# Kernel optimization log

Measured on AMD Instinct MI355X. Metric: run time of the kernel, lower is better.

The kernel has to match this reference:

```python
import jax, jax.numpy as jnp
import numpy as np

# module hyper-parameters (init_kwargs)
DELTA_VAR = 0.75
DELTA_DIST = 2.0
ALPHA, BETA, GAMMA = 1.0, 1.0, 0.001

B, E, H, W, C = 4, 16, 512, 512, 24


def _safe_norm(x, axis):
    # L2 norm with zero (not nan) gradient at 0, matching torch.norm's subgradient
    sq = jnp.sum(x * x, axis=axis)
    safe = jnp.where(sq == 0, 1.0, sq)
    return jnp.where(sq == 0, 0.0, jnp.sqrt(safe))


def setup_inputs() -> dict:
    key = jax.random.key(0)
    k1, k2 = jax.random.split(key)
    input_ = jax.random.normal(k1, (B, E, H, W), dtype=jnp.float32)
    target = jax.random.randint(k2, (B, 1, H, W), 0, C)  # consecutive labels 0..C-1 (w.h.p. all present)
    return {"input_": input_, "target": target, "n_instances": C}


def reference(input_, target, n_instances):
    # Discriminative loss (De Brabandere et al. 2017), math identical to the torch
    # one-hot-expansion version but expressed as segment reductions + gathers.
    Cn = int(n_instances)
    b, e = input_.shape[0], input_.shape[1]
    emb = input_.reshape(b, e, -1).transpose(0, 2, 1)  # (B, N, E)
    tgt = target.reshape(b, -1)                        # (B, N) int labels

    # per-instance cluster means: segment-sum over pixels (the torch code does the
    # same reduction via a dense BxCxExHxW one-hot expansion)
    def _means(e_bn, t_n):
        sums = jax.ops.segment_sum(e_bn, t_n, num_segments=Cn)                      # (C, E)
        counts = jax.ops.segment_sum(jnp.ones(t_n.shape, e_bn.dtype), t_n, num_segments=Cn)  # (C,)
        return sums / counts[:, None], counts

    mu, counts = jax.vmap(_means)(emb, tgt)            # (B, C, E), (B, C)

    # variance term: hinged distance of each pixel embedding to its own cluster mean
    mu_per_pix = jnp.take_along_axis(mu, tgt[:, :, None], axis=1)  # (B, N, E)
    dist = _safe_norm(emb - mu_per_pix, axis=-1)                   # (B, N)
    hinge = jnp.square(jnp.maximum(dist - DELTA_VAR, 0.0))
    var_per_inst = jax.vmap(lambda h, t: jax.ops.segment_sum(h, t, num_segments=Cn))(hinge, tgt) / counts  # (B, C)
    variance_term = jnp.mean(jnp.sum(var_per_inst, axis=1) / Cn)

    # distance term: hinged pairwise repulsion between cluster means
    dmat = _safe_norm(mu[:, :, None, :] - mu[:, None, :, :], axis=-1)  # (B, C, C)
    repulsion = 2.0 * DELTA_DIST * (1.0 - jnp.eye(Cn, dtype=mu.dtype))
    hinged = jnp.square(jnp.maximum(repulsion - dmat, 0.0))
    distance_term = jnp.mean(jnp.sum(hinged, axis=(1, 2))) / (Cn * (Cn - 1))

    # regularizer: mean norm of cluster means
    reg_term = jnp.mean(jnp.sum(_safe_norm(mu, axis=-1), axis=1)) / Cn

    return ALPHA * variance_term + BETA * distance_term + GAMMA * reg_term
```

## Files before the change

### kernel.cpp

```cpp
#include <hip/hip_runtime.h>
#include <cstdint>

#define B_SZ   4
#define E_DIM  16
#define C_INST 24
#define HW_N   262144
#define NG     (HW_N / 4)

#define DELTA_VAR  0.75f
#define DELTA_DIST 2.0f
#define ALPHA_W 1.0f
#define BETA_W  1.0f
#define GAMMA_W 0.001f

#define P1_NB   32
#define P1_ITER (NG / (P1_NB * 256))
#define CNT_PL  8
#define P2_BX   256
#define P2_TOTAL (P2_BX * B_SZ)

__global__ __launch_bounds__(256) void pass1_kernel(
    const float* __restrict__ input, const int* __restrict__ target,
    float* __restrict__ sums, float* __restrict__ counts)
{
    __shared__ float buk[C_INST][256];
    __shared__ float crow[4][C_INST];
    const int tid   = threadIdx.x;
    const int lane  = tid & 63;
    const int wv    = tid >> 6;
    const int chunk = blockIdx.x;
    const int eg    = blockIdx.y;
    const int b     = blockIdx.z;

    #pragma unroll
    for (int c = 0; c < C_INST; ++c) buk[c][tid] = 0.f;

    const int4* __restrict__ tgt4 = (const int4*)(target + (size_t)b * HW_N);
    const float4* __restrict__ src4 =
        (const float4*)(input + ((size_t)b * E_DIM + eg) * HW_N);
    const int gbase = chunk * 256 * P1_ITER + tid;

    int scnt[C_INST];
    #pragma unroll
    for (int c = 0; c < C_INST; ++c) scnt[c] = 0;

    int4   lab0 = tgt4[gbase];
    float4 x0   = src4[gbase];
    int4   lab1 = tgt4[gbase + 256];
    float4 x1   = src4[gbase + 256];
    #pragma unroll
    for (int it = 0; it < P1_ITER; ++it) {
        const int4   lc = lab0;
        const float4 xc = x0;
        lab0 = lab1; x0 = x1;
        if (it + 2 < P1_ITER) {
            lab1 = tgt4[gbase + (it + 2) * 256];
            x1   = src4[gbase + (it + 2) * 256];
        }
        buk[lc.x][tid] += xc.x;
        buk[lc.y][tid] += xc.y;
        buk[lc.z][tid] += xc.z;
        buk[lc.w][tid] += xc.w;
        if (eg < CNT_PL && it == eg) {
            #pragma unroll
            for (int c = 0; c < C_INST; ++c) {
                scnt[c] += (int)__popcll(__ballot(lc.x == c))
                         + (int)__popcll(__ballot(lc.y == c))
                         + (int)__popcll(__ballot(lc.z == c))
                         + (int)__popcll(__ballot(lc.w == c));
            }
        }
    }
    if (lane == 0) {
        #pragma unroll
        for (int c = 0; c < C_INST; ++c) crow[wv][c] = (float)scnt[c];
    }
    __syncthreads();

    if (tid < 8 * C_INST) {
        const int c  = tid >> 3;
        const int r0 = tid & 7;
        float s = 0.f;
        #pragma unroll
        for (int k = 0; k < 32; ++k)
            s += buk[c][r0 + 8 * ((k + c) & 31)];
        s += __shfl_xor(s, 1, 64);
        s += __shfl_xor(s, 2, 64);
        s += __shfl_xor(s, 4, 64);
        if (r0 == 0)
            unsafeAtomicAdd(&sums[((size_t)b * E_DIM + eg) * C_INST + c], s);
    }
    if (eg < CNT_PL && tid < C_INST) {
        const float s = crow[0][tid] + crow[1][tid] + crow[2][tid] + crow[3][tid];
        unsafeAtomicAdd(&counts[b * C_INST + tid], s);
    }
}

__global__ __launch_bounds__(256) void pass2_kernel(
    const float* __restrict__ input, const int* __restrict__ target,
    const float* __restrict__ sums, const float* __restrict__ counts,
    float* __restrict__ partials)
{
    __shared__ float4 mu4[C_INST][5];
    __shared__ float w_l[C_INST];
    __shared__ float redw[4];
    const int tid  = threadIdx.x;
    const int lane = tid & 63;
    const int wv   = tid >> 6;
    const int b    = blockIdx.y;

    if (tid < C_INST) {
        const float cv = counts[b * C_INST + tid];
        w_l[tid] = (cv > 0.f) ? 1.f / cv : 0.f;
    }
    __syncthreads();
    for (int i = tid; i < E_DIM * C_INST; i += 256) {
        const int e = i / C_INST, c = i % C_INST;
        ((float*)&mu4[c][0])[e] =
            sums[((size_t)b * E_DIM + e) * C_INST + c] * w_l[c];
    }
    __syncthreads();

    const int g = blockIdx.x * 256 + tid;
    const int4 lab4 = ((const int4*)(target + (size_t)b * HW_N))[g];
    const float4* __restrict__ src4 =
        (const float4*)(input + (size_t)b * E_DIM * NG * 4);

    float4 xv[E_DIM];
    #pragma unroll
    for (int e = 0; e < E_DIM; ++e)
        xv[e] = src4[(size_t)e * NG + g];

    float d2[4] = {0.f, 0.f, 0.f, 0.f};
    #pragma unroll
    for (int e4 = 0; e4 < 4; ++e4) {
        const float4 mx = mu4[lab4.x][e4];
        const float4 my = mu4[lab4.y][e4];
        const float4 mz = mu4[lab4.z][e4];
        const float4 mw = mu4[lab4.w][e4];
        float df;
        df = xv[4*e4+0].x - mx.x; d2[0] = fmaf(df, df, d2[0]);
        df = xv[4*e4+1].x - mx.y; d2[0] = fmaf(df, df, d2[0]);
        df = xv[4*e4+2].x - mx.z; d2[0] = fmaf(df, df, d2[0]);
        df = xv[4*e4+3].x - mx.w; d2[0] = fmaf(df, df, d2[0]);
        df = xv[4*e4+0].y - my.x; d2[1] = fmaf(df, df, d2[1]);
        df = xv[4*e4+1].y - my.y; d2[1] = fmaf(df, df, d2[1]);
        df = xv[4*e4+2].y - my.z; d2[1] = fmaf(df, df, d2[1]);
        df = xv[4*e4+3].y - my.w; d2[1] = fmaf(df, df, d2[1]);
        df = xv[4*e4+0].z - mz.x; d2[2] = fmaf(df, df, d2[2]);
        df = xv[4*e4+1].z - mz.y; d2[2] = fmaf(df, df, d2[2]);
        df = xv[4*e4+2].z - mz.z; d2[2] = fmaf(df, df, d2[2]);
        df = xv[4*e4+3].z - mz.w; d2[2] = fmaf(df, df, d2[2]);
        df = xv[4*e4+0].w - mw.x; d2[3] = fmaf(df, df, d2[3]);
        df = xv[4*e4+1].w - mw.y; d2[3] = fmaf(df, df, d2[3]);
        df = xv[4*e4+2].w - mw.z; d2[3] = fmaf(df, df, d2[3]);
        df = xv[4*e4+3].w - mw.w; d2[3] = fmaf(df, df, d2[3]);
    }

    float vloc = 0.f;
    {
        const int lp[4] = {lab4.x, lab4.y, lab4.z, lab4.w};
        #pragma unroll
        for (int p = 0; p < 4; ++p) {
            const float h = fmaxf(sqrtf(d2[p]) - DELTA_VAR, 0.f);
            vloc = fmaf(h * h, w_l[lp[p]], vloc);
        }
    }
    #pragma unroll
    for (int m = 1; m < 64; m <<= 1) vloc += __shfl_xor(vloc, m, 64);
    if (lane == 0) redw[wv] = vloc;
    __syncthreads();
    if (tid == 0)
        partials[b * P2_BX + blockIdx.x] = redw[0] + redw[1] + redw[2] + redw[3];
}

__global__ __launch_bounds__(256) void final_kernel(
    const float* __restrict__ sums, const float* __restrict__ counts,
    const float* __restrict__ partials, float* __restrict__ out)
{
    __shared__ float mu[B_SZ][C_INST][E_DIM];
    __shared__ float red[256];
    const int tid = threadIdx.x;

    for (int i = tid; i < B_SZ * C_INST * E_DIM; i += 256) {
        const int b = i / (C_INST * E_DIM);
        const int r = i % (C_INST * E_DIM);
        const int e = r / C_INST, c = r % C_INST;
        const float cv = counts[b * C_INST + c];
        mu[b][c][e] = (cv > 0.f)
            ? sums[((size_t)b * E_DIM + e) * C_INST + c] / cv : 0.f;
    }
    __syncthreads();

    float acc = 0.f;
    #pragma unroll
    for (int i = 0; i < P2_TOTAL / 256; ++i)
        acc += partials[i * 256 + tid] * (ALPHA_W / (B_SZ * C_INST));
    for (int i = tid; i < B_SZ * C_INST; i += 256) {
        const int b = i / C_INST, c = i % C_INST;
        float n2 = 0.f;
        #pragma unroll
        for (int e = 0; e < E_DIM; ++e) n2 += mu[b][c][e] * mu[b][c][e];
        acc += GAMMA_W * sqrtf(n2) * (1.0f / (B_SZ * C_INST));
    }
    for (int i = tid; i < B_SZ * C_INST * C_INST; i += 256) {
        const int b  = i / (C_INST * C_INST);
        const int r  = i % (C_INST * C_INST);
        const int c1 = r / C_INST, c2 = r % C_INST;
        if (c1 != c2) {
            float d2 = 0.f;
            #pragma unroll
            for (int e = 0; e < E_DIM; ++e) {
                const float d = mu[b][c1][e] - mu[b][c2][e];
                d2 += d * d;
            }
            const float h = fmaxf(2.0f * DELTA_DIST - sqrtf(d2), 0.f);
            acc += BETA_W * h * h * (1.0f / (B_SZ * C_INST * (C_INST - 1)));
        }
    }

    red[tid] = acc;
    __syncthreads();
    for (int s = 128; s > 0; s >>= 1) {
        if (tid < s) red[tid] += red[tid + s];
        __syncthreads();
    }
    if (tid == 0) out[0] = red[0];
}

extern "C" void kernel_launch(void* const* d_in, const int* in_sizes, int n_in,
                              void* d_out, int out_size, void* d_ws, size_t ws_size,
                              hipStream_t stream)
{
    const float* input  = (const float*)d_in[0];
    const int*   target = (const int*)d_in[1];

    float* sums     = (float*)d_ws;
    float* counts   = sums + B_SZ * E_DIM * C_INST;
    float* partials = counts + B_SZ * C_INST;
    const size_t ws_zero_bytes =
        (size_t)(B_SZ * E_DIM * C_INST + B_SZ * C_INST) * sizeof(float);
    hipMemsetAsync(d_ws, 0, ws_zero_bytes, stream);

    pass1_kernel<<<dim3(P1_NB, E_DIM, B_SZ), 256, 0, stream>>>(input, target, sums, counts);
    pass2_kernel<<<dim3(P2_BX, B_SZ), 256, 0, stream>>>(input, target, sums, counts, partials);
    final_kernel<<<1, 256, 0, stream>>>(sums, counts, partials, (float*)d_out);
}
```

Before: 119.2 us.

## Compute per-instance sums and counts with bf16 MFMA one-hot matmul

Pass1 is rewritten so that each block loads all 16 embedding channels for a pixel tile. It converts them to bf16 in LDS and accumulates the segment sums as a one-hot (label) by embedding matrix product on 32x32x16 bf16 MFMA, with a ones column producing the counts. This replaces the per-channel grid with LDS bucket scatter-adds and the ballot-based counting, and cuts the repeated label reads across 16 channel blocks. The cost is bf16 rounding of the embeddings in the cluster means, which may cost accuracy, plus extra LDS staging and two barriers per tile.

```diff
diff --git a/kernel.cpp b/kernel.cpp
--- a/kernel.cpp
+++ b/kernel.cpp
@@ -13,86 +13,105 @@
 #define BETA_W  1.0f
 #define GAMMA_W 0.001f
 
-#define P1_NB   32
-#define P1_ITER (NG / (P1_NB * 256))
-#define CNT_PL  8
+#define P1_CHUNKS 256
+#define P1_TILE   256
+#define P1_TILES  ((HW_N / P1_CHUNKS) / P1_TILE)
 #define P2_BX   256
 #define P2_TOTAL (P2_BX * B_SZ)
+
+typedef __attribute__((ext_vector_type(8)))  short bf16x8;
+typedef __attribute__((ext_vector_type(16))) float f32x16;
+
+__device__ __forceinline__ uint32_t bf16rne(float f) {
+    const uint32_t u = __float_as_uint(f);
+    return (u + 0x7FFFu + ((u >> 16) & 1u)) >> 16;
+}
 
 __global__ __launch_bounds__(256) void pass1_kernel(
     const float* __restrict__ input, const int* __restrict__ target,
     float* __restrict__ sums, float* __restrict__ counts)
 {
-    __shared__ float buk[C_INST][256];
-    __shared__ float crow[4][C_INST];
-    const int tid   = threadIdx.x;
-    const int lane  = tid & 63;
-    const int wv    = tid >> 6;
-    const int chunk = blockIdx.x;
-    const int eg    = blockIdx.y;
-    const int b     = blockIdx.z;
-
-    #pragma unroll
-    for (int c = 0; c < C_INST; ++c) buk[c][tid] = 0.f;
-
+    __shared__ unsigned short x_lds[E_DIM * 264];
+    __shared__ int   lab_lds[260];
+    __shared__ float racc[4][C_INST][18];
+
+    const int tid = threadIdx.x;
+    const int l   = tid & 63;
+    const int wv  = tid >> 6;
+    const int b   = blockIdx.y;
+
+    const float4* __restrict__ src4 =
+        (const float4*)(input + (size_t)b * E_DIM * HW_N);
     const int4* __restrict__ tgt4 = (const int4*)(target + (size_t)b * HW_N);
-    const float4* __restrict__ src4 =
-        (const float4*)(input + ((size_t)b * E_DIM + eg) * HW_N);
-    const int gbase = chunk * 256 * P1_ITER + tid;
-
-    int scnt[C_INST];
-    #pragma unroll
-    for (int c = 0; c < C_INST; ++c) scnt[c] = 0;
-
-    int4   lab0 = tgt4[gbase];
-    float4 x0   = src4[gbase];
-    int4   lab1 = tgt4[gbase + 256];
-    float4 x1   = src4[gbase + 256];
-    #pragma unroll
-    for (int it = 0; it < P1_ITER; ++it) {
-        const int4   lc = lab0;
-        const float4 xc = x0;
-        lab0 = lab1; x0 = x1;
-        if (it + 2 < P1_ITER) {
-            lab1 = tgt4[gbase + (it + 2) * 256];
-            x1   = src4[gbase + (it + 2) * 256];
-        }
-        buk[lc.x][tid] += xc.x;
-        buk[lc.y][tid] += xc.y;
-        buk[lc.z][tid] += xc.z;
-        buk[lc.w][tid] += xc.w;
-        if (eg < CNT_PL && it == eg) {
-            #pragma unroll
-            for (int c = 0; c < C_INST; ++c) {
-                scnt[c] += (int)__popcll(__ballot(lc.x == c))
-                         + (int)__popcll(__ballot(lc.y == c))
-                         + (int)__popcll(__ballot(lc.z == c))
-                         + (int)__popcll(__ballot(lc.w == c));
+    const int px_base = blockIdx.x << 10;
+
+    f32x16 acc;
+    #pragma unroll
+    for (int r = 0; r < 16; ++r) acc[r] = 0.f;
+
+    float4 xr[4];
+    int4   lr;
+    #define LOADT(t)  do {                                                   \
+        const int f4b = (px_base + (t) * P1_TILE) >> 2;                      \
+        _Pragma("unroll")                                                    \
+        for (int j = 0; j < 4; ++j)                                          \
+            xr[j] = src4[(size_t)(4 * j + wv) * NG + f4b + l];               \
+        if (tid < 64) lr = tgt4[f4b + tid];                                  \
+    } while (0)
+
+    LOADT(0);
+    for (int t = 0; t < P1_TILES; ++t) {
+        #pragma unroll
+        for (int j = 0; j < 4; ++j) {
+            uint2 p;
+            p.x = bf16rne(xr[j].x) | (bf16rne(xr[j].y) << 16);
+            p.y = bf16rne(xr[j].z) | (bf16rne(xr[j].w) << 16);
+            *(uint2*)&x_lds[(4 * j + wv) * 264 + l * 4] = p;
+        }
+        if (tid < 64) *(int4*)&lab_lds[tid * 4] = lr;
+        __syncthreads();
+        if (t + 1 < P1_TILES) LOADT(t + 1);
+
+        const int c = l & 31;
+        #pragma unroll
+        for (int m = 0; m < 4; ++m) {
+            const int k0 = wv * 64 + m * 16 + (l >> 5) * 8;
+            const int4 la = *(const int4*)&lab_lds[k0];
+            const int4 lb = *(const int4*)&lab_lds[k0 + 4];
+            union { uint32_t u[4]; bf16x8 v; } af;
+            af.u[0] = ((la.x == c) ? 0x3F80u : 0u) | ((la.y == c) ? 0x3F800000u : 0u);
+            af.u[1] = ((la.z == c) ? 0x3F80u : 0u) | ((la.w == c) ? 0x3F800000u : 0u);
+            af.u[2] = ((lb.x == c) ? 0x3F80u : 0u) | ((lb.y == c) ? 0x3F800000u : 0u);
+            af.u[3] = ((lb.z == c) ? 0x3F80u : 0u) | ((lb.w == c) ? 0x3F800000u : 0u);
+            union { uint32_t u[4]; bf16x8 v; } bf;
+            if (c < E_DIM) {
+                bf.v = *(const bf16x8*)&x_lds[c * 264 + k0];
+            } else if (c == E_DIM) {
+                bf.u[0] = bf.u[1] = bf.u[2] = bf.u[3] = 0x3F803F80u;
+            } else {
+                bf.u[0] = bf.u[1] = bf.u[2] = bf.u[3] = 0u;
             }
-        }
-    }
-    if (lane == 0) {
-        #pragma unroll
-        for (int c = 0; c < C_INST; ++c) crow[wv][c] = (float)scnt[c];
-    }
-    __syncthreads();
-
-    if (tid < 8 * C_INST) {
-        const int c  = tid >> 3;
-        const int r0 = tid & 7;
-        float s = 0.f;
-        #pragma unroll
-        for (int k = 0; k < 32; ++k)
-            s += buk[c][r0 + 8 * ((k + c) & 31)];
-        s += __shfl_xor(s, 1, 64);
-        s += __shfl_xor(s, 2, 64);
-        s += __shfl_xor(s, 4, 64);
-        if (r0 == 0)
-            unsafeAtomicAdd(&sums[((size_t)b * E_DIM + eg) * C_INST + c], s);
-    }
-    if (eg < CNT_PL && tid < C_INST) {
-        const float s = crow[0][tid] + crow[1][tid] + crow[2][tid] + crow[3][tid];
-        unsafeAtomicAdd(&counts[b * C_INST + tid], s);
+            acc = __builtin_amdgcn_mfma_f32_32x32x16_bf16(af.v, bf.v, acc, 0, 0, 0);
+        }
+        __syncthreads();
+    }
+    #undef LOADT
+
+    #pragma unroll
+    for (int r = 0; r < 16; ++r) {
+        const int row = (r & 3) + 8 * (r >> 2) + 4 * (l >> 5);
+        const int col = l & 31;
+        if (row < C_INST && col < 17) racc[wv][row][col] = acc[r];
+    }
+    __syncthreads();
+    for (int i = tid; i < C_INST * 17; i += 256) {
+        const int c = i / 17, e = i % 17;
+        const float s = racc[0][c][e] + racc[1][c][e]
+                      + racc[2][c][e] + racc[3][c][e];
+        if (e < E_DIM)
+            unsafeAtomicAdd(&sums[((size_t)b * E_DIM + e) * C_INST + c], s);
+        else
+            unsafeAtomicAdd(&counts[b * C_INST + c], s);
     }
 }
 
@@ -124,7 +143,7 @@
     const int g = blockIdx.x * 256 + tid;
     const int4 lab4 = ((const int4*)(target + (size_t)b * HW_N))[g];
     const float4* __restrict__ src4 =
-        (const float4*)(input + (size_t)b * E_DIM * NG * 4);
+        (const float4*)(input + (size_t)b * E_DIM * HW_N);
 
     float4 xv[E_DIM];
     #pragma unroll
@@ -242,7 +261,7 @@
         (size_t)(B_SZ * E_DIM * C_INST + B_SZ * C_INST) * sizeof(float);
     hipMemsetAsync(d_ws, 0, ws_zero_bytes, stream);
 
-    pass1_kernel<<<dim3(P1_NB, E_DIM, B_SZ), 256, 0, stream>>>(input, target, sums, counts);
+    pass1_kernel<<<dim3(P1_CHUNKS, B_SZ), 256, 0, stream>>>(input, target, sums, counts);
     pass2_kernel<<<dim3(P2_BX, B_SZ), 256, 0, stream>>>(input, target, sums, counts, partials);
     final_kernel<<<1, 256, 0, stream>>>(sums, counts, partials, (float*)d_out);
 }
```

New measurement: 150.7 us. 26.4% more time.
